# Kernel tuning notes

Hardware: AMD Instinct MI355X
Metric: run time of the kernel (lower is better)

Reference implementation:

```python
import jax, jax.numpy as jnp
import numpy as np

EPS = 1e-6


def setup_inputs() -> dict:
    key = jax.random.key(0)
    ks = jax.random.split(key, 7)
    b, n, d, H, hid = 4, 512, 128, 4, 32
    scale1 = 1.0 / np.sqrt(2 * d)
    scale2 = 1.0 / np.sqrt(hid)
    return {
        "x": jax.random.normal(ks[0], (b, n, d), dtype=jnp.float32),
        "W1": jax.random.normal(ks[1], (H, 2 * d, hid), dtype=jnp.float32) * scale1,
        "b1": jax.random.normal(ks[2], (H, hid), dtype=jnp.float32) * scale1,
        "W2": jax.random.normal(ks[3], (H, hid), dtype=jnp.float32) * scale2,
        "b2": jax.random.normal(ks[4], (H,), dtype=jnp.float32) * scale2,
        "Wp": jax.random.normal(ks[5], (d, d), dtype=jnp.float32) / np.sqrt(d),
        "bp": jax.random.normal(ks[6], (d,), dtype=jnp.float32) / np.sqrt(d),
    }


def reference(x, W1, b1, W2, b2, Wp, bp):
    # x: [b, n, d]; W1: [H, 2d, hid]; W2: [H, hid]
    d = x.shape[-1]
    # squared pairwise distance via gram matrix: ||xi - xj||^2
    sq = jnp.sum(x * x, axis=-1)                                   # [b, n]
    gram = jnp.einsum("bnd,bmd->bnm", x, x)                        # [b, n, n]
    dist2 = jnp.maximum(sq[:, :, None] + sq[:, None, :] - 2.0 * gram, 0.0)
    # per-head first linear on cat([xi, xj]) split into two projections
    ai = jnp.einsum("bnd,hdk->bhnk", x, W1[:, :d, :])              # [b, H, n, hid]
    aj = jnp.einsum("bnd,hdk->bhnk", x, W1[:, d:, :])              # [b, H, n, hid]
    pre = jnp.tanh(ai[:, :, :, None, :] + aj[:, :, None, :, :]
                   + b1[None, :, None, None, :])                   # [b, H, n, n, hid]
    sigma = jax.nn.softplus(jnp.einsum("bhnmk,hk->bhnm", pre, W2)
                            + b2[None, :, None, None])             # [b, H, n, n]
    adj = jnp.exp(-dist2[:, None, :, :] / (2.0 * sigma * sigma + EPS))
    adj_mean = jnp.mean(adj, axis=1)                               # [b, n, n]
    h = jnp.einsum("bnm,bmd->bnd", adj_mean, x)                    # [b, n, d]
    return h @ Wp + bp
```

## Files before the change

kernel.cpp:

```cpp
#include <hip/hip_runtime.h>

typedef float v4f __attribute__((ext_vector_type(4)));
typedef float v2f __attribute__((ext_vector_type(2)));

#define LOG2E  1.4426950408889634f
#define NLOG2E (-1.4426950408889634f)
#define C2L2E  2.8853900817779268f
#define LN2    0.6931471805599453f

__device__ __forceinline__ float fexp2(float x){ return __builtin_amdgcn_exp2f(x); }
__device__ __forceinline__ float flog2(float x){ return __builtin_amdgcn_logf(x); }
__device__ __forceinline__ float frcp (float x){ return __builtin_amdgcn_rcpf(x); }
__device__ __forceinline__ float hsum(v4f v){ return (v.x+v.y)+(v.z+v.w); }

__global__ __launch_bounds__(256) void prep_kernel(
    const float* __restrict__ x, const float* __restrict__ W1,
    const float* __restrict__ b1, const float* __restrict__ Wp,
    float* __restrict__ sq, float* __restrict__ Abuf,
    float* __restrict__ Bbuf, float* __restrict__ xpT)
{
  const int bid = blockIdx.x, t = threadIdx.x;
  if (bid >= 192) {
    int row = (bid - 192) * 256 + t;
    const v4f* xv = (const v4f*)(x + row * 128);
    float s = 0.f;
#pragma unroll
    for (int q = 0; q < 32; q++) { v4f v = xv[q]; s += hsum(v * v); }
    sq[row] = s;
    return;
  }
  __shared__ v4f Xs[64 * 9];
  __shared__ v4f Ws[32 * 16];
  const bool isAB = bid < 128;
  int it, ct;
  if (isAB) { it = bid >> 2; ct = bid & 3; }
  else      { int q = bid - 128; it = q >> 1; ct = q & 1; }
  const int row0 = it * 64;
  const int tx = t & 15, ty = t >> 4;
  const int r0 = ty * 4, c0 = tx * 4;
  v4f acc[4] = {};

  for (int dd0 = 0; dd0 < 128; dd0 += 32) {
    __syncthreads();
#pragma unroll
    for (int s2 = 0; s2 < 2; s2++) {
      int idx = t + s2 * 256;
      int row = idx >> 3, k4 = idx & 7;
      v4f v = *(const v4f*)(x + (row0 + row) * 128 + dd0 + k4 * 4);
      Xs[row * 9 + ((k4 + (row >> 2)) & 7)] = v;
    }
#pragma unroll
    for (int s2 = 0; s2 < 2; s2++) {
      int idx = t + s2 * 256;
      int dd = idx >> 4, cf4 = idx & 15;
      v4f v;
      if (isAB) {
        int cl = cf4 * 4; int half = cl >> 5; int k = cl & 31;
        v = *(const v4f*)(W1 + (ct * 256 + half * 128 + dd0 + dd) * 32 + k);
      } else {
        v = *(const v4f*)(Wp + (dd0 + dd) * 128 + ct * 64 + cf4 * 4);
      }
      Ws[dd * 16 + cf4] = v;
    }
    __syncthreads();
#pragma unroll
    for (int dd4 = 0; dd4 < 8; dd4++) {
      int sa = (dd4 + ty) & 7;
      v4f a0 = Xs[(r0 + 0) * 9 + sa], a1 = Xs[(r0 + 1) * 9 + sa];
      v4f a2 = Xs[(r0 + 2) * 9 + sa], a3 = Xs[(r0 + 3) * 9 + sa];
#pragma unroll
      for (int u = 0; u < 4; u++) {
        v4f bv = Ws[(dd4 * 4 + u) * 16 + tx];
        acc[0] += a0[u] * bv; acc[1] += a1[u] * bv;
        acc[2] += a2[u] * bv; acc[3] += a3[u] * bv;
      }
    }
  }

  if (isAB) {
    const int h = ct; const int half = c0 >> 5; const int k = c0 & 31;
    v4f bias = {};
    if (half == 0) bias = *(const v4f*)(b1 + h * 32 + k);
    float* dst = (half == 0) ? Abuf : Bbuf;
#pragma unroll
    for (int i = 0; i < 4; i++) {
      int rg = row0 + r0 + i; int b = rg >> 9; int ir = rg & 511;
      v4f o = (acc[i] + bias) * C2L2E;
      *(v4f*)(dst + ((b * 4 + h) * 512 + ir) * 32 + k) = o;
    }
  } else {
    int rg0 = row0 + r0; int b = rg0 >> 9; int ir0 = rg0 & 511;
#pragma unroll
    for (int u = 0; u < 4; u++) {
      int c = ct * 64 + c0 + u;
      v4f o = { acc[0][u], acc[1][u], acc[2][u], acc[3][u] };
      *(v4f*)(xpT + (b * 128 + c) * 512 + ir0) = o;
    }
  }
}

__global__ __launch_bounds__(256) void adj_kernel(
    const float* __restrict__ x, const float* __restrict__ sq,
    const float* __restrict__ Abuf, const float* __restrict__ Bbuf,
    const float* __restrict__ W2, const float* __restrict__ b2g,
    float* __restrict__ ADJ)
{
  const int jt = blockIdx.x, it = blockIdx.y, b = blockIdx.z;
  const int t = threadIdx.x, tx = t & 15, ty = t >> 4;
  const int r0 = 2 * ty, c0 = 2 * tx;
  __shared__ v4f As[32 * 9], Bs[32 * 9];
  __shared__ v4f W2s[32];
  __shared__ float hb[4];

  if (t < 32) W2s[t] = ((const v4f*)W2)[t];
  if (t < 4) {
    float s = b2g[t];
    for (int k = 0; k < 32; k++) s += W2[t * 32 + k];
    hb[t] = s;
  }

  const int row = t >> 3, k4l = t & 7, slot = (k4l + (row >> 1)) & 7;
  const float* xb = x + b * 512 * 128;

  v4f pa = *(const v4f*)(Abuf + ((size_t)((b * 4 + 0) * 512 + it * 32 + row)) * 32 + k4l * 4);
  v4f pb = *(const v4f*)(Bbuf + ((size_t)((b * 4 + 0) * 512 + jt * 32 + row)) * 32 + k4l * 4);

  v4f gacc[4] = {};
  for (int dd0 = 0; dd0 < 128; dd0 += 32) {
    __syncthreads();
    As[row * 9 + slot] = *(const v4f*)(xb + (it * 32 + row) * 128 + dd0 + k4l * 4);
    Bs[row * 9 + slot] = *(const v4f*)(xb + (jt * 32 + row) * 128 + dd0 + k4l * 4);
    __syncthreads();
#pragma unroll
    for (int k4 = 0; k4 < 8; k4++) {
      int sa = (k4 + ty) & 7, sb = (k4 + tx) & 7;
      v4f a0 = As[(r0 + 0) * 9 + sa], a1 = As[(r0 + 1) * 9 + sa];
      v4f b0 = Bs[(c0 + 0) * 9 + sb], b1v = Bs[(c0 + 1) * 9 + sb];
      gacc[0] += a0 * b0; gacc[1] += a0 * b1v;
      gacc[2] += a1 * b0; gacc[3] += a1 * b1v;
    }
  }
  float si0 = sq[b * 512 + it * 32 + r0], si1 = sq[b * 512 + it * 32 + r0 + 1];
  float sj0 = sq[b * 512 + jt * 32 + c0], sj1 = sq[b * 512 + jt * 32 + c0 + 1];
  float d2L[4] = {
    fmaxf(si0 + sj0 - 2.f * hsum(gacc[0]), 0.f) * NLOG2E,
    fmaxf(si0 + sj1 - 2.f * hsum(gacc[1]), 0.f) * NLOG2E,
    fmaxf(si1 + sj0 - 2.f * hsum(gacc[2]), 0.f) * NLOG2E,
    fmaxf(si1 + sj1 - 2.f * hsum(gacc[3]), 0.f) * NLOG2E };

  float accA[4] = {0.f, 0.f, 0.f, 0.f};
  for (int h = 0; h < 4; h++) {
    __syncthreads();
    As[row * 9 + slot] = pa;
    Bs[row * 9 + slot] = pb;
    __syncthreads();
    if (h < 3) {
      pa = *(const v4f*)(Abuf + ((size_t)((b * 4 + h + 1) * 512 + it * 32 + row)) * 32 + k4l * 4);
      pb = *(const v4f*)(Bbuf + ((size_t)((b * 4 + h + 1) * 512 + jt * 32 + row)) * 32 + k4l * 4);
    }
    float hbv = hb[h];
    float sacc[4] = { hbv, hbv, hbv, hbv };
#pragma unroll
    for (int k4 = 0; k4 < 8; k4++) {
      int sa = (k4 + ty) & 7, sb = (k4 + tx) & 7;
      v4f a0 = As[(r0 + 0) * 9 + sa], a1 = As[(r0 + 1) * 9 + sa];
      v4f b0 = Bs[(c0 + 0) * 9 + sb], b1v = Bs[(c0 + 1) * 9 + sb];
      v4f w2v = W2s[h * 8 + k4];
#pragma unroll
      for (int u = 0; u < 4; u++) {
        float wm = -2.f * w2v[u];
        float a0u = a0[u], a1u = a1[u], b0u = b0[u], b1u = b1v[u];
        float e;
        e = fexp2(a0u + b0u); sacc[0] = fmaf(wm, frcp(e + 1.f), sacc[0]);
        e = fexp2(a0u + b1u); sacc[1] = fmaf(wm, frcp(e + 1.f), sacc[1]);
        e = fexp2(a1u + b0u); sacc[2] = fmaf(wm, frcp(e + 1.f), sacc[2]);
        e = fexp2(a1u + b1u); sacc[3] = fmaf(wm, frcp(e + 1.f), sacc[3]);
      }
    }
#pragma unroll
    for (int p = 0; p < 4; p++) {
      float u2 = fexp2(sacc[p] * LOG2E);
      float sg = LN2 * flog2(1.f + u2);
      float den = fmaf(2.f * sg, sg, 1e-6f);
      accA[p] += fexp2(d2L[p] * frcp(den));
    }
  }
  float* dst = ADJ + ((size_t)(b * 512 + it * 32 + r0)) * 512 + jt * 32 + c0;
  v2f o0 = { accA[0] * 0.25f, accA[1] * 0.25f };
  v2f o1 = { accA[2] * 0.25f, accA[3] * 0.25f };
  *(v2f*)dst = o0;
  *(v2f*)(dst + 512) = o1;
}

__global__ __launch_bounds__(256) void out_kernel(
    const float* __restrict__ ADJ, const float* __restrict__ xpT,
    const float* __restrict__ bp, float* __restrict__ out)
{
  const int ct = blockIdx.x;
  const int it = blockIdx.y;
  const int b = blockIdx.z;
  const int t = threadIdx.x, tx = t & 15, ty = t >> 4;
  const int r0 = 2 * ty, c0 = 2 * tx;
  __shared__ v4f Ajs[32 * 9], Xps[32 * 9];
  v4f acc[4] = {};
  const int row = t >> 3, k4l = t & 7, slot = (k4l + (row >> 1)) & 7;

  for (int k0 = 0; k0 < 512; k0 += 32) {
    __syncthreads();
    Ajs[row * 9 + slot] = *(const v4f*)(ADJ + ((size_t)(b * 512 + it * 32 + row)) * 512 + k0 + k4l * 4);
    Xps[row * 9 + slot] = *(const v4f*)(xpT + ((size_t)(b * 128 + ct * 32 + row)) * 512 + k0 + k4l * 4);
    __syncthreads();
#pragma unroll
    for (int k4 = 0; k4 < 8; k4++) {
      int sa = (k4 + ty) & 7, sb = (k4 + tx) & 7;
      v4f a0 = Ajs[(r0 + 0) * 9 + sa], a1 = Ajs[(r0 + 1) * 9 + sa];
      v4f b0 = Xps[(c0 + 0) * 9 + sb], b1v = Xps[(c0 + 1) * 9 + sb];
      acc[0] += a0 * b0; acc[1] += a0 * b1v;
      acc[2] += a1 * b0; acc[3] += a1 * b1v;
    }
  }
  float bp0 = bp[ct * 32 + c0], bp1 = bp[ct * 32 + c0 + 1];
  float* dst = out + ((size_t)(b * 512 + it * 32 + r0)) * 128 + ct * 32 + c0;
  v2f o0 = { hsum(acc[0]) + bp0, hsum(acc[1]) + bp1 };
  v2f o1 = { hsum(acc[2]) + bp0, hsum(acc[3]) + bp1 };
  *(v2f*)dst = o0;
  *(v2f*)(dst + 128) = o1;
}

extern "C" void kernel_launch(void* const* d_in, const int* in_sizes, int n_in,
                              void* d_out, int out_size, void* d_ws, size_t ws_size,
                              hipStream_t stream) {
  const float* x  = (const float*)d_in[0];
  const float* W1 = (const float*)d_in[1];
  const float* b1 = (const float*)d_in[2];
  const float* W2 = (const float*)d_in[3];
  const float* b2 = (const float*)d_in[4];
  const float* Wp = (const float*)d_in[5];
  const float* bp = (const float*)d_in[6];
  float* out = (float*)d_out;

  float* ws  = (float*)d_ws;
  float* sq  = ws;
  float* A   = ws + 2048;
  float* Bb  = A + 262144;
  float* xpT = Bb + 262144;
  float* ADJ = xpT + 262144;

  prep_kernel<<<200, 256, 0, stream>>>(x, W1, b1, Wp, sq, A, Bb, xpT);
  adj_kernel<<<dim3(16, 16, 4), 256, 0, stream>>>(x, sq, A, Bb, W2, b2, ADJ);
  out_kernel<<<dim3(4, 16, 4), 256, 0, stream>>>(ADJ, xpT, bp, out);
}
```

Baseline: 67.44 us.

## Shrink adj tiles to 16x32, raise occupancy, split-K final GEMM

The adjacency kernel now computes a 16x32 tile per block, with each thread owning 1x2 outputs instead of 2x2. Two heads are staged per shared-memory load, and launch bounds are set to request 8 blocks per CU. This doubles the grid to give more waves and cut per-thread register pressure on the transcendental-heavy inner loop. The output GEMM is split along K into two halves that write partials, and a new reduce kernel adds them plus the bias. That extra launch and partial buffer trade some cost for more parallelism in a small GEMM.

```diff
diff --git a/kernel.cpp b/kernel.cpp
--- a/kernel.cpp
+++ b/kernel.cpp
@@ -99,7 +99,7 @@
   }
 }
 
-__global__ __launch_bounds__(256) void adj_kernel(
+__global__ __launch_bounds__(256, 8) void adj_kernel(
     const float* __restrict__ x, const float* __restrict__ sq,
     const float* __restrict__ Abuf, const float* __restrict__ Bbuf,
     const float* __restrict__ W2, const float* __restrict__ b2g,
@@ -107,8 +107,8 @@
 {
   const int jt = blockIdx.x, it = blockIdx.y, b = blockIdx.z;
   const int t = threadIdx.x, tx = t & 15, ty = t >> 4;
-  const int r0 = 2 * ty, c0 = 2 * tx;
-  __shared__ v4f As[32 * 9], Bs[32 * 9];
+  __shared__ v4f As[2 * 16 * 9];
+  __shared__ v4f Bs[2 * 32 * 9];
   __shared__ v4f W2s[32];
   __shared__ float hb[4];
 
@@ -119,93 +119,107 @@
     hb[t] = s;
   }
 
-  const int row = t >> 3, k4l = t & 7, slot = (k4l + (row >> 1)) & 7;
-  const float* xb = x + b * 512 * 128;
-
-  v4f pa = *(const v4f*)(Abuf + ((size_t)((b * 4 + 0) * 512 + it * 32 + row)) * 32 + k4l * 4);
-  v4f pb = *(const v4f*)(Bbuf + ((size_t)((b * 4 + 0) * 512 + jt * 32 + row)) * 32 + k4l * 4);
-
-  v4f gacc[4] = {};
-  for (int dd0 = 0; dd0 < 128; dd0 += 32) {
-    __syncthreads();
-    As[row * 9 + slot] = *(const v4f*)(xb + (it * 32 + row) * 128 + dd0 + k4l * 4);
-    Bs[row * 9 + slot] = *(const v4f*)(xb + (jt * 32 + row) * 128 + dd0 + k4l * 4);
-    __syncthreads();
-#pragma unroll
-    for (int k4 = 0; k4 < 8; k4++) {
-      int sa = (k4 + ty) & 7, sb = (k4 + tx) & 7;
-      v4f a0 = As[(r0 + 0) * 9 + sa], a1 = As[(r0 + 1) * 9 + sa];
-      v4f b0 = Bs[(c0 + 0) * 9 + sb], b1v = Bs[(c0 + 1) * 9 + sb];
-      gacc[0] += a0 * b0; gacc[1] += a0 * b1v;
-      gacc[2] += a1 * b0; gacc[3] += a1 * b1v;
-    }
-  }
-  float si0 = sq[b * 512 + it * 32 + r0], si1 = sq[b * 512 + it * 32 + r0 + 1];
-  float sj0 = sq[b * 512 + jt * 32 + c0], sj1 = sq[b * 512 + jt * 32 + c0 + 1];
-  float d2L[4] = {
-    fmaxf(si0 + sj0 - 2.f * hsum(gacc[0]), 0.f) * NLOG2E,
-    fmaxf(si0 + sj1 - 2.f * hsum(gacc[1]), 0.f) * NLOG2E,
-    fmaxf(si1 + sj0 - 2.f * hsum(gacc[2]), 0.f) * NLOG2E,
-    fmaxf(si1 + sj1 - 2.f * hsum(gacc[3]), 0.f) * NLOG2E };
-
-  float accA[4] = {0.f, 0.f, 0.f, 0.f};
-  for (int h = 0; h < 4; h++) {
-    __syncthreads();
-    As[row * 9 + slot] = pa;
-    Bs[row * 9 + slot] = pb;
-    __syncthreads();
-    if (h < 3) {
-      pa = *(const v4f*)(Abuf + ((size_t)((b * 4 + h + 1) * 512 + it * 32 + row)) * 32 + k4l * 4);
-      pb = *(const v4f*)(Bbuf + ((size_t)((b * 4 + h + 1) * 512 + jt * 32 + row)) * 32 + k4l * 4);
-    }
-    float hbv = hb[h];
-    float sacc[4] = { hbv, hbv, hbv, hbv };
-#pragma unroll
-    for (int k4 = 0; k4 < 8; k4++) {
-      int sa = (k4 + ty) & 7, sb = (k4 + tx) & 7;
-      v4f a0 = As[(r0 + 0) * 9 + sa], a1 = As[(r0 + 1) * 9 + sa];
-      v4f b0 = Bs[(c0 + 0) * 9 + sb], b1v = Bs[(c0 + 1) * 9 + sb];
-      v4f w2v = W2s[h * 8 + k4];
-#pragma unroll
-      for (int u = 0; u < 4; u++) {
-        float wm = -2.f * w2v[u];
-        float a0u = a0[u], a1u = a1[u], b0u = b0[u], b1u = b1v[u];
-        float e;
-        e = fexp2(a0u + b0u); sacc[0] = fmaf(wm, frcp(e + 1.f), sacc[0]);
-        e = fexp2(a0u + b1u); sacc[1] = fmaf(wm, frcp(e + 1.f), sacc[1]);
-        e = fexp2(a1u + b0u); sacc[2] = fmaf(wm, frcp(e + 1.f), sacc[2]);
-        e = fexp2(a1u + b1u); sacc[3] = fmaf(wm, frcp(e + 1.f), sacc[3]);
-      }
-    }
-#pragma unroll
-    for (int p = 0; p < 4; p++) {
-      float u2 = fexp2(sacc[p] * LOG2E);
-      float sg = LN2 * flog2(1.f + u2);
-      float den = fmaf(2.f * sg, sg, 1e-6f);
-      accA[p] += fexp2(d2L[p] * frcp(den));
-    }
-  }
-  float* dst = ADJ + ((size_t)(b * 512 + it * 32 + r0)) * 512 + jt * 32 + c0;
-  v2f o0 = { accA[0] * 0.25f, accA[1] * 0.25f };
-  v2f o1 = { accA[2] * 0.25f, accA[3] * 0.25f };
-  *(v2f*)dst = o0;
-  *(v2f*)(dst + 512) = o1;
-}
-
-__global__ __launch_bounds__(256) void out_kernel(
+  const int row0g = it * 16, col0g = jt * 32;
+  const int a_sec = t >> 7, a_row = (t >> 3) & 15, a_k4 = t & 7;
+  const int a_slot = (a_k4 + a_row) & 7;
+  const float* xb = x + (size_t)b * 512 * 128;
+
+  v4f gacc0 = {}, gacc1 = {};
+#pragma unroll
+  for (int half = 0; half < 2; half++) {
+    if (half) __syncthreads();
+    As[a_sec * 144 + a_row * 9 + a_slot] =
+      *(const v4f*)(xb + (row0g + a_row) * 128 + half * 64 + a_sec * 32 + a_k4 * 4);
+#pragma unroll
+    for (int s = 0; s < 2; s++) {
+      int idx = t + s * 256;
+      int sec = idx >> 8, col = (idx >> 3) & 31, k4 = idx & 7;
+      Bs[sec * 288 + col * 9 + ((k4 + (col >> 1)) & 7)] =
+        *(const v4f*)(xb + (col0g + col) * 128 + half * 64 + sec * 32 + k4 * 4);
+    }
+    __syncthreads();
+#pragma unroll
+    for (int c = 0; c < 2; c++) {
+#pragma unroll
+      for (int k4 = 0; k4 < 8; k4++) {
+        int sa = (k4 + ty) & 7, sb = (k4 + tx) & 7;
+        v4f a0 = As[c * 144 + ty * 9 + sa];
+        v4f b0 = Bs[c * 288 + (2 * tx) * 9 + sb];
+        v4f b1 = Bs[c * 288 + (2 * tx + 1) * 9 + sb];
+        gacc0 += a0 * b0; gacc1 += a0 * b1;
+      }
+    }
+  }
+  float si  = sq[b * 512 + row0g + ty];
+  float sj0 = sq[b * 512 + col0g + 2 * tx];
+  float sj1 = sq[b * 512 + col0g + 2 * tx + 1];
+  float d2L0 = fmaxf(si + sj0 - 2.f * hsum(gacc0), 0.f) * NLOG2E;
+  float d2L1 = fmaxf(si + sj1 - 2.f * hsum(gacc1), 0.f) * NLOG2E;
+
+  float acc0 = 0.f, acc1 = 0.f;
+#pragma unroll
+  for (int g = 0; g < 2; g++) {
+    __syncthreads();
+    As[a_sec * 144 + a_row * 9 + a_slot] =
+      *(const v4f*)(Abuf + ((size_t)((b * 4 + g * 2 + a_sec) * 512 + row0g + a_row)) * 32 + a_k4 * 4);
+#pragma unroll
+    for (int s = 0; s < 2; s++) {
+      int idx = t + s * 256;
+      int sec = idx >> 8, col = (idx >> 3) & 31, k4 = idx & 7;
+      Bs[sec * 288 + col * 9 + ((k4 + (col >> 1)) & 7)] =
+        *(const v4f*)(Bbuf + ((size_t)((b * 4 + g * 2 + sec) * 512 + col0g + col)) * 32 + k4 * 4);
+    }
+    __syncthreads();
+#pragma unroll
+    for (int hh = 0; hh < 2; hh++) {
+      int h = g * 2 + hh;
+      float hbv = hb[h];
+      float s0 = hbv, s1 = hbv;
+#pragma unroll
+      for (int k4 = 0; k4 < 8; k4++) {
+        int sa = (k4 + ty) & 7, sb = (k4 + tx) & 7;
+        v4f a0 = As[hh * 144 + ty * 9 + sa];
+        v4f b0 = Bs[hh * 288 + (2 * tx) * 9 + sb];
+        v4f b1 = Bs[hh * 288 + (2 * tx + 1) * 9 + sb];
+        v4f w2v = W2s[h * 8 + k4];
+#pragma unroll
+        for (int u = 0; u < 4; u++) {
+          float wm = -2.f * w2v[u];
+          float au = a0[u];
+          float e0 = fexp2(au + b0[u]);
+          s0 = fmaf(wm, frcp(e0 + 1.f), s0);
+          float e1 = fexp2(au + b1[u]);
+          s1 = fmaf(wm, frcp(e1 + 1.f), s1);
+        }
+      }
+      float u20 = fexp2(s0 * LOG2E);
+      float sg0 = LN2 * flog2(1.f + u20);
+      float den0 = fmaf(2.f * sg0, sg0, 1e-6f);
+      acc0 += fexp2(d2L0 * frcp(den0));
+      float u21 = fexp2(s1 * LOG2E);
+      float sg1 = LN2 * flog2(1.f + u21);
+      float den1 = fmaf(2.f * sg1, sg1, 1e-6f);
+      acc1 += fexp2(d2L1 * frcp(den1));
+    }
+  }
+  v2f o = { acc0 * 0.25f, acc1 * 0.25f };
+  *(v2f*)(ADJ + ((size_t)(b * 512 + row0g + ty)) * 512 + col0g + 2 * tx) = o;
+}
+
+__global__ __launch_bounds__(256) void out_gemm(
     const float* __restrict__ ADJ, const float* __restrict__ xpT,
-    const float* __restrict__ bp, float* __restrict__ out)
+    float* __restrict__ part)
 {
   const int ct = blockIdx.x;
   const int it = blockIdx.y;
-  const int b = blockIdx.z;
+  const int z = blockIdx.z; const int b = z >> 1, ks = z & 1;
   const int t = threadIdx.x, tx = t & 15, ty = t >> 4;
   const int r0 = 2 * ty, c0 = 2 * tx;
   __shared__ v4f Ajs[32 * 9], Xps[32 * 9];
   v4f acc[4] = {};
   const int row = t >> 3, k4l = t & 7, slot = (k4l + (row >> 1)) & 7;
 
-  for (int k0 = 0; k0 < 512; k0 += 32) {
+  for (int k0 = ks * 256; k0 < ks * 256 + 256; k0 += 32) {
     __syncthreads();
     Ajs[row * 9 + slot] = *(const v4f*)(ADJ + ((size_t)(b * 512 + it * 32 + row)) * 512 + k0 + k4l * 4);
     Xps[row * 9 + slot] = *(const v4f*)(xpT + ((size_t)(b * 128 + ct * 32 + row)) * 512 + k0 + k4l * 4);
@@ -219,12 +233,22 @@
       acc[2] += a1 * b0; acc[3] += a1 * b1v;
     }
   }
-  float bp0 = bp[ct * 32 + c0], bp1 = bp[ct * 32 + c0 + 1];
-  float* dst = out + ((size_t)(b * 512 + it * 32 + r0)) * 128 + ct * 32 + c0;
-  v2f o0 = { hsum(acc[0]) + bp0, hsum(acc[1]) + bp1 };
-  v2f o1 = { hsum(acc[2]) + bp0, hsum(acc[3]) + bp1 };
+  float* dst = part + ((size_t)((ks * 4 + b) * 512 + it * 32 + r0)) * 128 + ct * 32 + c0;
+  v2f o0 = { hsum(acc[0]), hsum(acc[1]) };
+  v2f o1 = { hsum(acc[2]), hsum(acc[3]) };
   *(v2f*)dst = o0;
   *(v2f*)(dst + 128) = o1;
+}
+
+__global__ __launch_bounds__(256) void reduce_out(
+    const float* __restrict__ part, const float* __restrict__ bp,
+    float* __restrict__ out)
+{
+  int g = blockIdx.x * 256 + threadIdx.x;
+  const v4f* p = (const v4f*)part;
+  v4f s = p[g] + p[g + 65536];
+  v4f bv = ((const v4f*)bp)[g & 31];
+  ((v4f*)out)[g] = s + bv;
 }
 
 extern "C" void kernel_launch(void* const* d_in, const int* in_sizes, int n_in,
@@ -245,8 +269,10 @@
   float* Bb  = A + 262144;
   float* xpT = Bb + 262144;
   float* ADJ = xpT + 262144;
+  float* part = ADJ + 1048576;
 
   prep_kernel<<<200, 256, 0, stream>>>(x, W1, b1, Wp, sq, A, Bb, xpT);
-  adj_kernel<<<dim3(16, 16, 4), 256, 0, stream>>>(x, sq, A, Bb, W2, b2, ADJ);
-  out_kernel<<<dim3(4, 16, 4), 256, 0, stream>>>(ADJ, xpT, bp, out);
-}
+  adj_kernel<<<dim3(16, 32, 4), 256, 0, stream>>>(x, sq, A, Bb, W2, b2, ADJ);
+  out_gemm<<<dim3(4, 16, 8), 256, 0, stream>>>(ADJ, xpT, part);
+  reduce_out<<<256, 256, 0, stream>>>(part, bp, out);
+}
```

Result: slower. 206.3 us (+205.9%).
